# Kernel optimization log

Measured on AMD Instinct MI355X. Metric: run time of the kernel, lower is better.

The kernel has to match this reference:

```python
import jax, jax.numpy as jnp
import numpy as np

N = 100000   # nodes
E = 1600000  # edges
D = 128      # feature dim
C = 32       # n classes (logits dim)
LN_EPS = 1e-5   # torch LayerNorm default eps
LOG_EPS = 1e-9  # numerical floor inside logs


def setup_inputs() -> dict:
    key = jax.random.key(0)
    ks = jax.random.split(key, 8)
    h = jax.random.normal(ks[0], (N, D), jnp.float32)
    logits = jax.random.normal(ks[1], (N, C), jnp.float32)
    old_z = jax.random.uniform(ks[2], (N,), jnp.float32)
    norm = jax.random.uniform(ks[3], (N, 1), jnp.float32)  # degree norm per node
    tau_1 = jax.random.uniform(ks[4], (1,), jnp.float32)
    tau_2 = jax.random.uniform(ks[5], (1,), jnp.float32)
    src = jax.random.randint(ks[6], (E,), 0, N, jnp.int32)
    dst = jax.random.randint(ks[7], (E,), 0, N, jnp.int32)
    return dict(h=h, logits=logits, old_z=old_z, norm=norm,
                tau_1=tau_1, tau_2=tau_2, src=src, dst=dst)


def _layernorm_over_nodes(x):
    # LayerNorm(N, elementwise_affine=False) applied to a length-N vector:
    # normalize over the entire node dimension.
    mu = jnp.mean(x)
    var = jnp.mean(jnp.square(x - mu))
    return (x - mu) * jax.lax.rsqrt(var + LN_EPS)


def reference(h, logits, old_z, norm, tau_1, tau_2, src, dst):
    # --- message pass 1: adaptive_reduce_func over neighbor logits ---
    probs = jax.nn.softmax(logits, axis=-1)                      # [N,C]
    ones = jnp.ones((src.shape[0],), h.dtype)
    deg = jax.ops.segment_sum(ones, dst, num_segments=N)          # in-degree [N]
    sum_p = jax.ops.segment_sum(probs[src], dst, num_segments=N)  # [N,C]
    mean_p = sum_p / jnp.maximum(deg, 1.0)[:, None]               # neighborhood consensus
    log_self = jnp.log(probs + LOG_EPS)
    log_mean = jnp.log(mean_p + LOG_EPS)
    f1 = jnp.sum(probs * (log_self - log_mean), axis=-1)          # KL(self || mean-neighbor)
    f2 = -jnp.sum(mean_p * log_mean, axis=-1)                     # entropy of consensus
    has_nb = deg > 0  # DGL leaves zero-in-degree nodes at 0
    f1 = jnp.where(has_nb, f1, 0.0)
    f2 = jnp.where(has_nb, f2, 0.0)

    # --- gating (shared_tau=True path) ---
    z = jax.nn.sigmoid(-(_layernorm_over_nodes(f1) - tau_1)) \
      * jax.nn.sigmoid(-(_layernorm_over_nodes(f2) - tau_2))      # [N]
    gate = jnp.minimum(old_z, z)

    # --- message pass 2: sum-aggregate neighbor features ---
    agg = jax.ops.segment_sum(h[src], dst, num_segments=N)        # [N,D]
    normagg = jax.nn.relu(agg * norm)
    new_h = h + gate[:, None] * normagg
    return new_h, z
```

## Files before the change

kernel.cpp:

```cpp
#include <hip/hip_runtime.h>
#include <math.h>

#define CN 32
#define DN 128
#define BKT_SHIFT 9
#define BKT_NODES 512
#define CHUNK 8192
#define MAXBKT 1024
#define DCAP 12288
#define NSLICE 4

__global__ void k_sm_hist(const int* __restrict__ dst, int* __restrict__ M,
                          const float* __restrict__ logits, float* __restrict__ probs,
                          int E, int NBKT, int NCH, int N) {
    if ((int)blockIdx.x < NCH) {
        __shared__ int hist[MAXBKT];
        int t = threadIdx.x;
        for (int j = t; j < NBKT; j += 256) hist[j] = 0;
        __syncthreads();
        int ebeg = blockIdx.x * CHUNK;
        #pragma unroll
        for (int k = 0; k < CHUNK / 256; ++k) {
            int e = ebeg + k * 256 + t;
            if (e < E) atomicAdd(&hist[dst[e] >> BKT_SHIFT], 1);
        }
        __syncthreads();
        int* row = M + (size_t)blockIdx.x * NBKT;
        for (int j = t; j < NBKT; j += 256) row[j] = hist[j];
    } else {
        int t = (blockIdx.x - NCH) * blockDim.x + threadIdx.x;
        int node = t >> 5, c = t & 31;
        if (node >= N) return;
        float l = logits[node * CN + c];
        float m = l;
        #pragma unroll
        for (int o = 16; o; o >>= 1) m = fmaxf(m, __shfl_xor(m, o, 32));
        float e = __expf(l - m);
        float s = e;
        #pragma unroll
        for (int o = 16; o; o >>= 1) s += __shfl_xor(s, o, 32);
        probs[node * CN + c] = e / s;
    }
}

__global__ void k_scan_a(int* __restrict__ M, int* __restrict__ bsum, int NCH, int NBKT) {
    int b = blockIdx.x;
    int t = threadIdx.x, ln = t & 63, wv = t >> 6;
    int v = (t < NCH) ? M[(size_t)t * NBKT + b] : 0;
    int incl = v;
    #pragma unroll
    for (int o = 1; o < 64; o <<= 1) { int u = __shfl_up(incl, o, 64); if (ln >= o) incl += u; }
    __shared__ int wsum[4], wpre[4];
    if (ln == 63) wsum[wv] = incl;
    __syncthreads();
    if (t == 0) {
        int r = 0;
        for (int w = 0; w < 4; ++w) { wpre[w] = r; r += wsum[w]; }
    }
    __syncthreads();
    int excl = wpre[wv] + incl - v;
    if (t < NCH) M[(size_t)t * NBKT + b] = excl;
    if (t == 255) bsum[b] = excl + v;
}

__global__ void k_scan_b(const int* __restrict__ bsum, int* __restrict__ bbase, int NBKT, int E) {
    int t = threadIdx.x, ln = t & 63, wv = t >> 6;
    int v = (t < NBKT) ? bsum[t] : 0;
    int incl = v;
    #pragma unroll
    for (int o = 1; o < 64; o <<= 1) { int u = __shfl_up(incl, o, 64); if (ln >= o) incl += u; }
    __shared__ int wsum[4], wpre[4];
    if (ln == 63) wsum[wv] = incl;
    __syncthreads();
    if (t == 0) {
        int r = 0;
        for (int w = 0; w < 4; ++w) { wpre[w] = r; r += wsum[w]; }
    }
    __syncthreads();
    if (t < NBKT) bbase[t] = wpre[wv] + incl - v;
    if (t == 0) bbase[NBKT] = E;
}

__global__ void k_part_scatter(const int* __restrict__ src, const int* __restrict__ dst,
                               const int* __restrict__ M, const int* __restrict__ bbase,
                               int* __restrict__ part, int E, int NBKT) {
    __shared__ int cur[MAXBKT];
    int t = threadIdx.x;
    const int* row = M + (size_t)blockIdx.x * NBKT;
    for (int j = t; j < NBKT; j += 256) cur[j] = row[j] + bbase[j];
    __syncthreads();
    int ebeg = blockIdx.x * CHUNK;
    #pragma unroll
    for (int k = 0; k < CHUNK / 256; ++k) {
        int e = ebeg + k * 256 + t;
        if (e < E) {
            int d = dst[e];
            int b = d >> BKT_SHIFT;
            int p = atomicAdd(&cur[b], 1);
            part[p] = ((d & (BKT_NODES - 1)) << 17) | src[e];
        }
    }
}

__global__ void k_bucket_csr(int* __restrict__ part, const int* __restrict__ bbase,
                             int* __restrict__ cnt, int* __restrict__ off, int N) {
    __shared__ int sbuf[DCAP];
    __shared__ int hcnt[BKT_NODES];
    __shared__ int wsum[8], wpre[8];
    int t = threadIdx.x, ln = t & 63, wv = t >> 6;
    int b = blockIdx.x;
    int lo = bbase[b], hi = bbase[b + 1];
    int n = hi - lo;
    if (n > DCAP) n = DCAP;
    for (int e = t; e < n; e += BKT_NODES) sbuf[e] = part[lo + e];
    hcnt[t] = 0;
    __syncthreads();
    for (int e = t; e < n; e += BKT_NODES) atomicAdd(&hcnt[sbuf[e] >> 17], 1);
    __syncthreads();
    int v = hcnt[t];
    int incl = v;
    #pragma unroll
    for (int o = 1; o < 64; o <<= 1) { int u = __shfl_up(incl, o, 64); if (ln >= o) incl += u; }
    if (ln == 63) wsum[wv] = incl;
    __syncthreads();
    if (t == 0) {
        int r = 0;
        #pragma unroll
        for (int w = 0; w < 8; ++w) { wpre[w] = r; r += wsum[w]; }
    }
    __syncthreads();
    int excl = wpre[wv] + incl - v;
    int g = b * BKT_NODES + t;
    if (g < N) { cnt[g] = v; off[g] = lo + excl; }
    hcnt[t] = excl;
    __syncthreads();
    for (int e = t; e < n; e += BKT_NODES) {
        int pk = sbuf[e];
        int p = atomicAdd(&hcnt[pk >> 17], 1);
        part[lo + p] = pk & 0x1FFFF;
    }
}

__global__ void k_fused(const float* __restrict__ probs, const int* __restrict__ off,
                        const int* __restrict__ cnt, const int* __restrict__ eidx,
                        float* __restrict__ f1buf, float* __restrict__ f2buf,
                        double* __restrict__ pbuf,
                        const float* __restrict__ h, float* __restrict__ aggout,
                        int N, int NGS, int NBF) {
    const int HB = NSLICE * NGS;
    if ((int)blockIdx.x < HB) {
        int slice = blockIdx.x / NGS;
        int g = (blockIdx.x - slice * NGS) * 16 + (threadIdx.x >> 4);
        int c = threadIdx.x & 15;
        if (g >= N) return;
        int beg = off[g], dg = cnt[g];
        const float2* h2 = (const float2*)h;
        size_t coloff = (size_t)slice * 16 + c;
        float ax = 0.f, ay = 0.f;
        for (int base = 0; base < dg; base += 16) {
            int rem = dg - base;
            int lim = rem < 16 ? rem : 16;
            int myi = (c < lim) ? __builtin_nontemporal_load(&eidx[beg + base + c]) : 0;
            #pragma unroll
            for (int j = 0; j < 16; ++j) {
                int s = __shfl(myi, j, 16);
                float2 v = h2[(size_t)s * 64 + coloff];
                bool use = j < rem;
                ax += use ? v.x : 0.f;
                ay += use ? v.y : 0.f;
            }
        }
        float* op = (float*)&((float2*)aggout)[(size_t)g * 64 + coloff];
        __builtin_nontemporal_store(ax, op);
        __builtin_nontemporal_store(ay, op + 1);
    } else {
        int pb = blockIdx.x - HB;
        int t = pb * blockDim.x + threadIdx.x;
        int i = t >> 5, c = t & 31;
        float f1 = 0.f, f2 = 0.f;
        if (i < N) {
            int beg = off[i], dg = cnt[i];
            float sum = 0.f;
            for (int base = 0; base < dg; base += 16) {
                int rem = dg - base;
                int lim = rem < 16 ? rem : 16;
                int myi = (c < lim) ? __builtin_nontemporal_load(&eidx[beg + base + c]) : 0;
                #pragma unroll
                for (int j = 0; j < 16; ++j) {
                    int s = __shfl(myi, j, 32);
                    float v = probs[(size_t)s * CN + c];
                    sum += (j < rem) ? v : 0.f;
                }
            }
            float f1c = 0.f, f2c = 0.f;
            if (dg > 0) {
                float p = probs[(size_t)i * CN + c];
                float mp = sum / (float)dg;
                float lm = logf(mp + 1e-9f);
                f1c = p * (logf(p + 1e-9f) - lm);
                f2c = -mp * lm;
            }
            #pragma unroll
            for (int o = 16; o; o >>= 1) { f1c += __shfl_xor(f1c, o, 32); f2c += __shfl_xor(f2c, o, 32); }
            if (c == 0) { f1buf[i] = f1c; f2buf[i] = f2c; f1 = f1c; f2 = f2c; }
        }
        double v0 = f1, v1 = (double)f1 * f1, v2 = f2, v3 = (double)f2 * f2;
        #pragma unroll
        for (int o = 32; o; o >>= 1) {
            v0 += __shfl_down(v0, o, 64);
            v1 += __shfl_down(v1, o, 64);
            v2 += __shfl_down(v2, o, 64);
            v3 += __shfl_down(v3, o, 64);
        }
        __shared__ double sh[4][4];
        int wave = threadIdx.x >> 6, lane = threadIdx.x & 63;
        if (lane == 0) { sh[0][wave] = v0; sh[1][wave] = v1; sh[2][wave] = v2; sh[3][wave] = v3; }
        __syncthreads();
        if (threadIdx.x == 0) {
            double a = 0, b = 0, c2 = 0, d = 0;
            #pragma unroll
            for (int w = 0; w < 4; ++w) { a += sh[0][w]; b += sh[1][w]; c2 += sh[2][w]; d += sh[3][w]; }
            double* p = pbuf + (size_t)pb * 4;
            p[0] = a; p[1] = b; p[2] = c2; p[3] = d;
        }
    }
}

__global__ void k_redstats(const double* __restrict__ pbuf, double* __restrict__ stats, int nblk) {
    int t = threadIdx.x;
    double a = 0, b = 0, c = 0, d = 0;
    for (int k = t; k < nblk; k += blockDim.x) {
        const double* p = pbuf + (size_t)k * 4;
        a += p[0]; b += p[1]; c += p[2]; d += p[3];
    }
    #pragma unroll
    for (int o = 32; o; o >>= 1) {
        a += __shfl_down(a, o, 64);
        b += __shfl_down(b, o, 64);
        c += __shfl_down(c, o, 64);
        d += __shfl_down(d, o, 64);
    }
    __shared__ double sh[4][16];
    int wv = t >> 6, ln = t & 63;
    if (ln == 0) { sh[0][wv] = a; sh[1][wv] = b; sh[2][wv] = c; sh[3][wv] = d; }
    __syncthreads();
    if (t == 0) {
        double s0 = 0, s1 = 0, s2 = 0, s3 = 0;
        int nw = blockDim.x >> 6;
        for (int w = 0; w < nw; ++w) { s0 += sh[0][w]; s1 += sh[1][w]; s2 += sh[2][w]; s3 += sh[3][w]; }
        stats[0] = s0; stats[1] = s1; stats[2] = s2; stats[3] = s3;
    }
}

__global__ void k_z_ep(const float* __restrict__ f1buf, const float* __restrict__ f2buf,
                       const double* __restrict__ stats, const float* __restrict__ old_z,
                       const float* __restrict__ tau1, const float* __restrict__ tau2,
                       const float* __restrict__ h, const float* __restrict__ norm,
                       float* __restrict__ out, float* __restrict__ z_out, int N) {
    int t = blockIdx.x * blockDim.x + threadIdx.x;
    int i = t >> 5, c = t & 31;
    if (i >= N) return;
    double invN = 1.0 / (double)N;
    float mu1 = (float)(stats[0] * invN);
    float var1 = (float)(stats[1] * invN) - mu1 * mu1;
    float is1 = rsqrtf(var1 + 1e-5f);
    float mu2 = (float)(stats[2] * invN);
    float var2 = (float)(stats[3] * invN) - mu2 * mu2;
    float is2 = rsqrtf(var2 + 1e-5f);
    float a = (f1buf[i] - mu1) * is1;
    float b = (f2buf[i] - mu2) * is2;
    float z = (1.f / (1.f + __expf(a - tau1[0]))) * (1.f / (1.f + __expf(b - tau2[0])));
    if (c == 0) z_out[i] = z;
    float g = fminf(old_z[i], z);
    float nm = norm[i];
    float4 av = ((const float4*)out)[(size_t)i * 32 + c];
    float4 hv = ((const float4*)h)[(size_t)i * 32 + c];
    float4 r;
    r.x = hv.x + g * fmaxf(av.x * nm, 0.f);
    r.y = hv.y + g * fmaxf(av.y * nm, 0.f);
    r.z = hv.z + g * fmaxf(av.z * nm, 0.f);
    r.w = hv.w + g * fmaxf(av.w * nm, 0.f);
    ((float4*)out)[(size_t)i * 32 + c] = r;
}

extern "C" void kernel_launch(void* const* d_in, const int* in_sizes, int n_in,
                              void* d_out, int out_size, void* d_ws, size_t ws_size,
                              hipStream_t stream) {
    const float* h      = (const float*)d_in[0];
    const float* logits = (const float*)d_in[1];
    const float* old_z  = (const float*)d_in[2];
    const float* norm   = (const float*)d_in[3];
    const float* tau1   = (const float*)d_in[4];
    const float* tau2   = (const float*)d_in[5];
    const int*   src    = (const int*)d_in[6];
    const int*   dst    = (const int*)d_in[7];
    const int N = in_sizes[2];
    const int E = in_sizes[6];

    float* out   = (float*)d_out;
    float* z_out = out + (size_t)N * DN;

    const int B = 256;
    const int NBF  = (N * CN + B - 1) / B;
    const int NGS  = (N + 15) / 16;
    const int NBKT = (N + BKT_NODES - 1) >> BKT_SHIFT;
    const int NCH  = (E + CHUNK - 1) / CHUNK;

    char*   ws    = (char*)d_ws;
    double* stats = (double*)ws;
    int*    cnt   = (int*)(ws + 64);
    int*    off   = cnt + N;
    int*    bbase = off + N;
    int*    bsum  = bbase + MAXBKT + 8;
    int*    M     = bsum + MAXBKT;
    int*    eidx  = M + (size_t)NCH * NBKT;
    float*  probs = (float*)(eidx + E);
    float*  f1buf = probs + (size_t)N * CN;
    float*  f2buf = f1buf + N;
    double* pbuf  = (double*)(((size_t)(f2buf + N) + 15) & ~(size_t)15);

    k_sm_hist<<<NCH + NBF, B, 0, stream>>>(dst, M, logits, probs, E, NBKT, NCH, N);
    k_scan_a<<<NBKT, 256, 0, stream>>>(M, bsum, NCH, NBKT);
    k_scan_b<<<1, 256, 0, stream>>>(bsum, bbase, NBKT, E);
    k_part_scatter<<<NCH, 256, 0, stream>>>(src, dst, M, bbase, eidx, E, NBKT);
    k_bucket_csr<<<NBKT, BKT_NODES, 0, stream>>>(eidx, bbase, cnt, off, N);

    k_fused<<<NSLICE * NGS + NBF, B, 0, stream>>>(probs, off, cnt, eidx, f1buf, f2buf, pbuf,
                                                  h, out, N, NGS, NBF);
    k_redstats<<<1, 1024, 0, stream>>>(pbuf, stats, NBF);
    k_z_ep<<<(N * 32 + B - 1) / B, B, 0, stream>>>(f1buf, f2buf, stats, old_z, tau1, tau2,
                                                   h, norm, out, z_out, N);
}
```

Measured before the change: 249.0 us.

## Aggregate full feature rows per wavefront with float4 loads and early loop exit

The neighbor-feature aggregation now gives each node one 64-lane wavefront instead of four column slices of 16 lanes. The wavefront is split into two halves that each gather alternating neighbors as float4 loads, and the halves are combined with a cross-half shuffle. Both gather loops now exit as soon as they pass the real neighbor count instead of running all 16 masked iterations. This reads eidx and off/cnt once per node rather than four times and skips wasted loads for low-degree nodes. The cost is the added shuffle reduction and that half the lanes sit idle during the store.

```diff
diff --git a/kernel.cpp b/kernel.cpp
--- a/kernel.cpp
+++ b/kernel.cpp
@@ -8,7 +8,6 @@
 #define CHUNK 8192
 #define MAXBKT 1024
 #define DCAP 12288
-#define NSLICE 4
 
 __global__ void k_sm_hist(const int* __restrict__ dst, int* __restrict__ M,
                           const float* __restrict__ logits, float* __restrict__ probs,
@@ -146,35 +145,45 @@
                         float* __restrict__ f1buf, float* __restrict__ f2buf,
                         double* __restrict__ pbuf,
                         const float* __restrict__ h, float* __restrict__ aggout,
-                        int N, int NGS, int NBF) {
-    const int HB = NSLICE * NGS;
-    if ((int)blockIdx.x < HB) {
-        int slice = blockIdx.x / NGS;
-        int g = (blockIdx.x - slice * NGS) * 16 + (threadIdx.x >> 4);
-        int c = threadIdx.x & 15;
-        if (g >= N) return;
-        int beg = off[g], dg = cnt[g];
-        const float2* h2 = (const float2*)h;
-        size_t coloff = (size_t)slice * 16 + c;
-        float ax = 0.f, ay = 0.f;
-        for (int base = 0; base < dg; base += 16) {
+                        int N, int NH, int NBF) {
+    if ((int)blockIdx.x < NH) {
+        int t = blockIdx.x * blockDim.x + threadIdx.x;
+        int i = t >> 6, ln = t & 63;
+        if (i >= N) return;
+        int half = ln >> 5, q = ln & 31;
+        int beg = off[i], dg = cnt[i];
+        const float4* h4 = (const float4*)h;
+        float ax = 0.f, ay = 0.f, az = 0.f, aw = 0.f;
+        for (int base = 0; base < dg; base += 32) {
             int rem = dg - base;
-            int lim = rem < 16 ? rem : 16;
-            int myi = (c < lim) ? __builtin_nontemporal_load(&eidx[beg + base + c]) : 0;
+            int lim = rem < 32 ? rem : 32;
+            int myi = (ln < lim) ? __builtin_nontemporal_load(&eidx[beg + base + ln]) : 0;
             #pragma unroll
             for (int j = 0; j < 16; ++j) {
-                int s = __shfl(myi, j, 16);
-                float2 v = h2[(size_t)s * 64 + coloff];
-                bool use = j < rem;
+                if ((j << 1) >= lim) break;
+                int nb = (j << 1) + half;
+                int s = __shfl(myi, nb, 64);
+                float4 v = h4[(size_t)s * 32 + q];
+                bool use = nb < lim;
                 ax += use ? v.x : 0.f;
                 ay += use ? v.y : 0.f;
+                az += use ? v.z : 0.f;
+                aw += use ? v.w : 0.f;
             }
         }
-        float* op = (float*)&((float2*)aggout)[(size_t)g * 64 + coloff];
-        __builtin_nontemporal_store(ax, op);
-        __builtin_nontemporal_store(ay, op + 1);
+        ax += __shfl_xor(ax, 32, 64);
+        ay += __shfl_xor(ay, 32, 64);
+        az += __shfl_xor(az, 32, 64);
+        aw += __shfl_xor(aw, 32, 64);
+        if (half == 0) {
+            float* op = (float*)&((float4*)aggout)[(size_t)i * 32 + q];
+            __builtin_nontemporal_store(ax, op);
+            __builtin_nontemporal_store(ay, op + 1);
+            __builtin_nontemporal_store(az, op + 2);
+            __builtin_nontemporal_store(aw, op + 3);
+        }
     } else {
-        int pb = blockIdx.x - HB;
+        int pb = blockIdx.x - NH;
         int t = pb * blockDim.x + threadIdx.x;
         int i = t >> 5, c = t & 31;
         float f1 = 0.f, f2 = 0.f;
@@ -187,9 +196,10 @@
                 int myi = (c < lim) ? __builtin_nontemporal_load(&eidx[beg + base + c]) : 0;
                 #pragma unroll
                 for (int j = 0; j < 16; ++j) {
+                    if (j >= lim) break;
                     int s = __shfl(myi, j, 32);
                     float v = probs[(size_t)s * CN + c];
-                    sum += (j < rem) ? v : 0.f;
+                    sum += v;
                 }
             }
             float f1c = 0.f, f2c = 0.f;
@@ -302,7 +312,7 @@
 
     const int B = 256;
     const int NBF  = (N * CN + B - 1) / B;
-    const int NGS  = (N + 15) / 16;
+    const int NH   = (N + 3) / 4;
     const int NBKT = (N + BKT_NODES - 1) >> BKT_SHIFT;
     const int NCH  = (E + CHUNK - 1) / CHUNK;
 
@@ -325,8 +335,8 @@
     k_part_scatter<<<NCH, 256, 0, stream>>>(src, dst, M, bbase, eidx, E, NBKT);
     k_bucket_csr<<<NBKT, BKT_NODES, 0, stream>>>(eidx, bbase, cnt, off, N);
 
-    k_fused<<<NSLICE * NGS + NBF, B, 0, stream>>>(probs, off, cnt, eidx, f1buf, f2buf, pbuf,
-                                                  h, out, N, NGS, NBF);
+    k_fused<<<NH + NBF, B, 0, stream>>>(probs, off, cnt, eidx, f1buf, f2buf, pbuf,
+                                        h, out, N, NH, NBF);
     k_redstats<<<1, 1024, 0, stream>>>(pbuf, stats, NBF);
     k_z_ep<<<(N * 32 + B - 1) / B, B, 0, stream>>>(f1buf, f2buf, stats, old_z, tau1, tau2,
                                                    h, norm, out, z_out, N);
```

New measurement: 276.4 us. +11.0%, slower.
